# Performance work log

Hardware: AMD Instinct MI355X
Metric: run time of the kernel (lower is better)

## Reference

```python
import jax, jax.numpy as jnp
import numpy as np

QDEPTH = 20
WIDTH = HEIGHT = 28
PIXELS = WIDTH * HEIGHT          # 784
WIRES = 10                        # ceil(log2(784))
BATCH = 8192


def setup_inputs() -> dict:
    key = jax.random.key(0)
    k1, k2, k3, k4 = jax.random.split(key, 4)
    x = jax.random.normal(k1, (BATCH, 1, WIDTH, HEIGHT), jnp.float32)
    W = jax.random.normal(k2, (WIRES, PIXELS), jnp.float32) / np.sqrt(PIXELS)
    b = jax.random.normal(k3, (WIRES,), jnp.float32) * 0.01
    qweights = jax.random.normal(k4, (QDEPTH, WIRES, 3), jnp.float32) * 0.4
    return {"x": x, "W": W, "b": b, "qweights": qweights}


def _apply_1q(state, gate, wire):
    """Apply a single-qubit gate. state: (B,)+(2,)*WIRES; gate: (2,2) or (B,2,2)."""
    ax = 1 + wire
    s = jnp.moveaxis(state, ax, 1)
    shp = s.shape
    s = s.reshape(shp[0], 2, -1)
    if gate.ndim == 2:
        s = jnp.einsum('ij,bjr->bir', gate, s)
    else:
        s = jnp.einsum('bij,bjr->bir', gate, s)
    return jnp.moveaxis(s.reshape(shp), 1, ax)


def _cnot(state, c, t):
    """CNOT with control c, target t on state (B,)+(2,)*WIRES."""
    s = jnp.moveaxis(state, (1 + c, 1 + t), (1, 2))
    # when control==1, flip target axis
    s = jnp.concatenate([s[:, :1], jnp.flip(s[:, 1:2], axis=2)], axis=1)
    return jnp.moveaxis(s, (1, 2), (1 + c, 1 + t))


def _ry_batched(theta):
    """theta: (B,) -> (B,2,2) complex RY gates."""
    c = jnp.cos(theta / 2)
    s = jnp.sin(theta / 2)
    g = jnp.stack([jnp.stack([c, -s], -1), jnp.stack([s, c], -1)], -2)
    return g.astype(jnp.complex64)


def _rot(phi, theta, omega):
    """PennyLane Rot(phi,theta,omega) = RZ(omega) RY(theta) RZ(phi), scalars -> (2,2)."""
    c = jnp.cos(theta / 2)
    s = jnp.sin(theta / 2)
    m00 = jnp.exp(-0.5j * (phi + omega)) * c
    m01 = -jnp.exp(0.5j * (phi - omega)) * s
    m10 = jnp.exp(-0.5j * (phi - omega)) * s
    m11 = jnp.exp(0.5j * (phi + omega)) * c
    return jnp.stack([jnp.stack([m00, m01]), jnp.stack([m10, m11])]).astype(jnp.complex64)


def _forward(x, W, b, qweights):
    B = x.shape[0]
    feat = x.reshape(B, -1)                       # b 1 w h -> b (w h)
    angles = feat @ W.T + b                       # linear_down -> (B, WIRES)

    # |0...0> statevector, wire 0 most significant (PennyLane convention)
    state = jnp.zeros((B,) + (2,) * WIRES, jnp.complex64)
    state = state.at[(slice(None),) + (0,) * WIRES].set(1.0)

    # AngleEmbedding, rotation='Y'
    for w in range(WIRES):
        state = _apply_1q(state, _ry_batched(angles[:, w]), w)

    # StronglyEntanglingLayers: per-layer Rot on every wire, then CNOT ring
    for l in range(QDEPTH):
        for w in range(WIRES):
            state = _apply_1q(state, _rot(qweights[l, w, 0], qweights[l, w, 1], qweights[l, w, 2]), w)
        r = (l % (WIRES - 1)) + 1                 # default PennyLane ranges
        for w in range(WIRES):
            state = _cnot(state, w, (w + r) % WIRES)

    sv = state.reshape(B, -1)
    probs = sv.real ** 2 + sv.imag ** 2           # qml.probs over all wires
    out = jnp.clip(probs[:, :PIXELS] * PIXELS, 0.0, 1.0)
    return out.reshape(B, 1, WIDTH, HEIGHT)


def reference(x, W, b, qweights):
    return _forward(x, W, b, qweights)
```

## Files before the change

kernel.cpp:

```cpp
#include <hip/hip_runtime.h>
#include <hip/hip_bf16.h>
#include <stdint.h>


#define NWIRES  10
#define DIM     1024
#define NLAYERS 20
#define NGATES  200
#define NPASS   100
#define PIXELS  784
#define BATCH   8192

typedef _Float16 f16;
typedef _Float16 f16x8 __attribute__((ext_vector_type(8)));
typedef float    f32x4 __attribute__((ext_vector_type(4)));
typedef float    f32x2 __attribute__((ext_vector_type(2)));

typedef const __attribute__((address_space(1))) void* gas1_t;
typedef __attribute__((address_space(3))) void*       las3_t;

__device__ __forceinline__ void gload_lds16(const void* g, void* l) {
  __builtin_amdgcn_global_load_lds((gas1_t)g, (las3_t)l, 16, 0, 0);
}

__global__ __launch_bounds__(256) void k_prep(const float* __restrict__ qw,
                                              float* __restrict__ plan_mat,
                                              unsigned* __restrict__ plan_idx,
                                              unsigned* __restrict__ plan_final) {
  __shared__ float gm[NGATES][8];
  const int tid = threadIdx.x;

  if (tid < NGATES) {
    float phi = qw[tid * 3 + 0], th = qw[tid * 3 + 1], om = qw[tid * 3 + 2];
    float s, c, sa, ca, sb, cb;
    sincosf(0.5f * th, &s, &c);
    sincosf(0.5f * (phi + om), &sa, &ca);
    sincosf(0.5f * (phi - om), &sb, &cb);
    gm[tid][0] = ca * c;  gm[tid][1] = sa * c;
    gm[tid][2] = cb * s;  gm[tid][3] = sb * s;
    gm[tid][4] = -cb * s; gm[tid][5] = sb * s;
    gm[tid][6] = ca * c;  gm[tid][7] = -sa * c;
  }
  __syncthreads();

  if (tid == 0) {
    unsigned rowA[NWIRES], invc[NWIRES];
    for (int i = 0; i < NWIRES; i++) { rowA[i] = 1u << i; invc[i] = 1u << i; }
    for (int lrev = 0; lrev < NLAYERS; lrev++) {
      int l = NLAYERS - 1 - lrev;
      int r = (l % (NWIRES - 1)) + 1;
      for (int w = NWIRES - 1; w >= 0; w--) {
        int c = w, t = (w + r) % NWIRES;
        int pc = 9 - c, pt = 9 - t;
        rowA[pt] ^= rowA[pc];
        invc[pc] ^= invc[pt];
      }
      for (int s = 0; s < 5; s++) {
        int w1 = 2 * s, w2 = 2 * s + 1;
        int p1 = 9 - w1, p2 = 9 - w2;
        unsigned u1 = rowA[p1], u2 = rowA[p2];
        unsigned m1 = invc[p1], m2 = invc[p2];
        unsigned b1 = u1 & (0u - u1);
        if (u2 & b1) u2 ^= u1;
        unsigned b2 = u2 & (0u - u2);
        if (u1 & b2) u1 ^= u2;
        unsigned bLo = (b1 < b2) ? b1 : b2;
        unsigned bHi = (b1 < b2) ? b2 : b1;
        unsigned* P = plan_idx + (size_t)(lrev * 5 + s) * 8;
        P[0] = bLo; P[1] = bHi; P[2] = u1; P[3] = u2;
        P[4] = b1;  P[5] = b2;  P[6] = m1; P[7] = m2;
      }
    }
    for (int p = 0; p < NWIRES; p++) plan_final[p] = invc[p];
  } else if (tid >= 100 && tid < 200) {
    int t = tid - 100;
    int lrev = t / 5, s = t % 5;
    int l = NLAYERS - 1 - lrev;
    int g1 = l * NWIRES + 2 * s, g2 = g1 + 1;
    float* K = plan_mat + (size_t)t * 64;
#pragma unroll
    for (int r = 0; r < 4; r++) {
#pragma unroll
      for (int c = 0; c < 4; c++) {
        int r1 = r >> 1, c1 = c >> 1, r2 = r & 1, c2 = c & 1;
        float ar = gm[g1][(r1 * 2 + c1) * 2], ai = gm[g1][(r1 * 2 + c1) * 2 + 1];
        float br = gm[g2][(r2 * 2 + c2) * 2], bi = gm[g2][(r2 * 2 + c2) * 2 + 1];
        float kr = ar * br - ai * bi;
        float ki = ar * bi + ai * br;
        float* e = K + (r * 4 + c) * 4;
        e[0] = kr; e[1] = kr; e[2] = -ki; e[3] = ki;
      }
    }
  }
}

__global__ __launch_bounds__(256) void k_main(const float* __restrict__ plan_mat,
                                              const unsigned* __restrict__ plan_idx,
                                              const unsigned* __restrict__ plan_final,
                                              const float* __restrict__ x,
                                              const float* __restrict__ W,
                                              const float* __restrict__ bias,
                                              f16* __restrict__ E,
                                              f16* __restrict__ Bt) {
  __shared__ f32x2 st[DIM];
  __shared__ float part[4][NWIRES];
  __shared__ float csh[NWIRES][2];

  const int tid = threadIdx.x;

  if (blockIdx.x < PIXELS) {
    const int col = blockIdx.x;

    for (int i = tid; i < DIM; i += 256)
      st[i] = (f32x2){i == col ? 1.f : 0.f, 0.f};
    __syncthreads();

    for (int t = 0; t < NPASS; t++) {
      const unsigned* P = plan_idx + (size_t)t * 8;
      const unsigned bLo = P[0], bHi = P[1], u1 = P[2], u2 = P[3];
      const unsigned pb1 = P[4], pb2 = P[5], m1 = P[6], m2 = P[7];
      const f32x4* Kp = (const f32x4*)(plan_mat + (size_t)t * 64);

      unsigned q  = (unsigned)tid;
      unsigned xx = ((q & ~(bLo - 1u)) << 1) | (q & (bLo - 1u));
      unsigned j0 = ((xx & ~(bHi - 1u)) << 1) | (xx & (bHi - 1u));
      unsigned j  = j0 ^ ((__popc(u1 & j0) & 1) ? pb1 : 0u)
                       ^ ((__popc(u2 & j0) & 1) ? pb2 : 0u);

      f32x2 v0 = st[j];
      f32x2 v1 = st[j ^ m2];
      f32x2 v2 = st[j ^ m1];
      f32x2 v3 = st[j ^ m1 ^ m2];
      f32x2 w0 = {v0.y, v0.x}, w1 = {v1.y, v1.x};
      f32x2 w2 = {v2.y, v2.x}, w3 = {v3.y, v3.x};

      f32x2 r0 = {0.f, 0.f}, r1 = {0.f, 0.f}, r2 = {0.f, 0.f}, r3 = {0.f, 0.f};
#define CM(rr, e, vv, ww)                         \
      { f32x4 kk = Kp[e];                         \
        rr += (f32x2){kk.x, kk.y} * (vv);         \
        rr += (f32x2){kk.z, kk.w} * (ww); }
      CM(r0, 0, v0, w0)  CM(r0, 1, v1, w1)  CM(r0, 2, v2, w2)  CM(r0, 3, v3, w3)
      CM(r1, 4, v0, w0)  CM(r1, 5, v1, w1)  CM(r1, 6, v2, w2)  CM(r1, 7, v3, w3)
      CM(r2, 8, v0, w0)  CM(r2, 9, v1, w1)  CM(r2, 10, v2, w2) CM(r2, 11, v3, w3)
      CM(r3, 12, v0, w0) CM(r3, 13, v1, w1) CM(r3, 14, v2, w2) CM(r3, 15, v3, w3)
#undef CM

      __syncthreads();
      st[j]           = r0;
      st[j ^ m2]      = r1;
      st[j ^ m1]      = r2;
      st[j ^ m1 ^ m2] = r3;
      __syncthreads();
    }

    unsigned invl[NWIRES];
#pragma unroll
    for (int p = 0; p < NWIRES; p++) invl[p] = plan_final[p];

    __align__(8) f16 re4[4], im4[4];
#pragma unroll
    for (int u = 0; u < 4; u++) {
      int i = tid * 4 + u;
      unsigned j = 0;
#pragma unroll
      for (int p = 0; p < NWIRES; p++)
        if ((i >> p) & 1) j ^= invl[p];
      f32x2 v = st[j];
      re4[u] = (f16)v.x;
      im4[u] = (f16)(-v.y);
    }
    *(uint2*)(&Bt[(size_t)(2 * col) * DIM + tid * 4])     = *(const uint2*)re4;
    *(uint2*)(&Bt[(size_t)(2 * col + 1) * DIM + tid * 4]) = *(const uint2*)im4;
    return;
  }

  const int b = blockIdx.x - PIXELS;
  const float* xr = x + (size_t)b * PIXELS;

  float acc[NWIRES];
#pragma unroll
  for (int w = 0; w < NWIRES; w++) acc[w] = 0.f;

  for (int k = tid; k < PIXELS; k += 256) {
    float xv = xr[k];
#pragma unroll
    for (int w = 0; w < NWIRES; w++) acc[w] = fmaf(xv, W[w * PIXELS + k], acc[w]);
  }

#pragma unroll
  for (int w = 0; w < NWIRES; w++) {
    float v = acc[w];
#pragma unroll
    for (int off = 32; off > 0; off >>= 1) v += __shfl_xor(v, off, 64);
    acc[w] = v;
  }

  const int wv = tid >> 6, ln = tid & 63;
  if (ln == 0) {
#pragma unroll
    for (int w = 0; w < NWIRES; w++) part[wv][w] = acc[w];
  }
  __syncthreads();
  if (tid < NWIRES) {
    float a = part[0][tid] + part[1][tid] + part[2][tid] + part[3][tid] + bias[tid];
    float s, c;
    sincosf(0.5f * a, &s, &c);
    csh[tid][0] = c;
    csh[tid][1] = s;
  }
  __syncthreads();

  __align__(8) f16 e4[4];
#pragma unroll
  for (int u = 0; u < 4; u++) {
    int i = tid * 4 + u;
    float pr = 1.f;
#pragma unroll
    for (int w = 0; w < NWIRES; w++) pr *= csh[w][(i >> (9 - w)) & 1];
    e4[u] = (f16)pr;
  }
  *(uint2*)(&E[(size_t)b * DIM + tid * 4]) = *(const uint2*)e4;
}

__global__ __launch_bounds__(256) void k_gemm(const f16* __restrict__ E,
                                              const f16* __restrict__ Bt,
                                              float* __restrict__ out) {
  __shared__ __align__(16) f16 As[128 * 64];
  __shared__ __align__(16) f16 Bs[128 * 64];

  const int tid = threadIdx.x;
  const int wv = tid >> 6, ln = tid & 63;
  const int wr = wv >> 1, wc = wv & 1;

  const int bid = blockIdx.x;
  const int swz = (bid & 7) * 104 + (bid >> 3);
  const int mt  = swz / 13, nt = swz % 13;
  const int m0  = mt * 128;
  const int n0  = nt * 128;

  f32x4 acc[4][4];
#pragma unroll
  for (int a = 0; a < 4; a++)
#pragma unroll
    for (int q = 0; q < 4; q++) acc[a][q] = (f32x4){0.f, 0.f, 0.f, 0.f};

  for (int kt = 0; kt < 16; kt++) {
#pragma unroll
    for (int r = 0; r < 4; r++) {
      int ub  = (r * 4 + wv) * 64;
      int u   = ub + ln;
      int row = u >> 3;
      int cb  = (u & 7) * 16;
      const char* gA = (const char*)E  + ((size_t)(m0 + row) * 2048) + kt * 128 + cb;
      const char* gB = (const char*)Bt + ((size_t)(n0 + row) * 2048) + kt * 128 + cb;
      gload_lds16(gA, (char*)As + (size_t)ub * 16);
      gload_lds16(gB, (char*)Bs + (size_t)ub * 16);
    }
    __syncthreads();

#pragma unroll
    for (int ks = 0; ks < 2; ks++) {
      f16x8 af[4], bf[4];
#pragma unroll
      for (int mi = 0; mi < 4; mi++)
        af[mi] = *(const f16x8*)&As[(wr * 64 + mi * 16 + (ln & 15)) * 64 + ks * 32 + (ln >> 4) * 8];
#pragma unroll
      for (int ni = 0; ni < 4; ni++)
        bf[ni] = *(const f16x8*)&Bs[(wc * 64 + ni * 16 + (ln & 15)) * 64 + ks * 32 + (ln >> 4) * 8];
#pragma unroll
      for (int mi = 0; mi < 4; mi++)
#pragma unroll
        for (int ni = 0; ni < 4; ni++)
          acc[mi][ni] = __builtin_amdgcn_mfma_f32_16x16x32_f16(af[mi], bf[ni], acc[mi][ni], 0, 0, 0);
    }
    __syncthreads();
  }

#pragma unroll
  for (int mi = 0; mi < 4; mi++) {
#pragma unroll
    for (int ni = 0; ni < 4; ni++) {
      int nbase = n0 + wc * 64 + ni * 16 + (ln & 15);
      int p = nbase >> 1;
      bool even = (ln & 1) == 0;
#pragma unroll
      for (int r = 0; r < 4; r++) {
        float v = acc[mi][ni][r];
        float o = __shfl_xor(v, 1, 64);
        if (even && p < PIXELS) {
          int m = m0 + wr * 64 + mi * 16 + (ln >> 4) * 4 + r;
          float s2 = (v * v + o * o) * (float)PIXELS;
          out[(size_t)m * PIXELS + p] = fminf(fmaxf(s2, 0.f), 1.f);
        }
      }
    }
  }
}

extern "C" void kernel_launch(void* const* d_in, const int* in_sizes, int n_in,
                              void* d_out, int out_size, void* d_ws, size_t ws_size,
                              hipStream_t stream) {
  const float* x    = (const float*)d_in[0];
  const float* W    = (const float*)d_in[1];
  const float* bias = (const float*)d_in[2];
  const float* qw   = (const float*)d_in[3];
  float* out        = (float*)d_out;

  char* ws = (char*)d_ws;
  f16* E  = (f16*)(ws);
  f16* Bt = (f16*)(ws + (size_t)16 * 1024 * 1024);
  float*    plan_mat   = (float*)(ws + (size_t)20 * 1024 * 1024);
  unsigned* plan_idx   = (unsigned*)(ws + (size_t)20 * 1024 * 1024 + 65536);
  unsigned* plan_final = (unsigned*)(ws + (size_t)20 * 1024 * 1024 + 131072);

  k_prep<<<dim3(1), dim3(256), 0, stream>>>(qw, plan_mat, plan_idx, plan_final);
  k_main<<<dim3(PIXELS + BATCH), dim3(256), 0, stream>>>(plan_mat, plan_idx,
                                                         plan_final, x, W, bias,
                                                         E, Bt);
  k_gemm<<<dim3(832), dim3(256), 0, stream>>>(E, Bt, out);
}
```

Baseline: 146.7 us.

## Retile GEMM to double-buffered 256x256 tiles and drop redundant gate-loop barrier

Rewrites the probability GEMM to use 256x256 output tiles with 512 threads. It double-buffers the global-to-LDS loads so the next K slice streams in while MFMAs run, and raises MFMA wave priority during the compute phase. It also removes one __syncthreads in the gate-application loop of k_main, relying on each thread owning a disjoint group of four amplitudes. The larger tiles cut global traffic per FLOP, but the grid shrinks to 224 blocks (fewer than the CU count) at 128KB of LDS per block, and the N range now reads padded Bt rows that are masked out at store.

Result: faster. 143.1 us (-2.5%).

```diff
diff --git a/kernel.cpp b/kernel.cpp
--- a/kernel.cpp
+++ b/kernel.cpp
@@ -145,7 +145,6 @@
       CM(r3, 12, v0, w0) CM(r3, 13, v1, w1) CM(r3, 14, v2, w2) CM(r3, 15, v3, w3)
 #undef CM
 
-      __syncthreads();
       st[j]           = r0;
       st[j ^ m2]      = r1;
       st[j ^ m1]      = r2;
@@ -222,73 +221,91 @@
   *(uint2*)(&E[(size_t)b * DIM + tid * 4]) = *(const uint2*)e4;
 }
 
-__global__ __launch_bounds__(256) void k_gemm(const f16* __restrict__ E,
-                                              const f16* __restrict__ Bt,
-                                              float* __restrict__ out) {
-  __shared__ __align__(16) f16 As[128 * 64];
-  __shared__ __align__(16) f16 Bs[128 * 64];
+__device__ __forceinline__ void g_stage(const f16* __restrict__ g, f16* l,
+                                        int tid, int row0, int kt) {
+#pragma unroll
+  for (int r = 0; r < 4; r++) {
+    int u = r * 512 + tid;
+    int row = u >> 3, c8 = u & 7;
+    gload_lds16((const char*)g + (size_t)(row0 + row) * 2048 + kt * 128 + c8 * 16,
+                (char*)l + (size_t)u * 16);
+  }
+}
+
+__global__ __launch_bounds__(512, 2) void k_gemm(const f16* __restrict__ E,
+                                                 const f16* __restrict__ Bt,
+                                                 float* __restrict__ out) {
+  __shared__ __align__(16) f16 As[2][256 * 64];
+  __shared__ __align__(16) f16 Bs[2][256 * 64];
 
   const int tid = threadIdx.x;
-  const int wv = tid >> 6, ln = tid & 63;
-  const int wr = wv >> 1, wc = wv & 1;
+  const int wid = tid >> 6, ln = tid & 63;
+  const int wm = wid >> 2, wn = wid & 3;
 
   const int bid = blockIdx.x;
-  const int swz = (bid & 7) * 104 + (bid >> 3);
-  const int mt  = swz / 13, nt = swz % 13;
-  const int m0  = mt * 128;
-  const int n0  = nt * 128;
-
-  f32x4 acc[4][4];
-#pragma unroll
-  for (int a = 0; a < 4; a++)
+  const int swz = (bid & 7) * 28 + (bid >> 3);
+  const int mt  = swz % 32, nt = swz / 32;
+  const int m0  = mt * 256;
+  const int n0  = nt * 256;
+
+  f32x4 acc[8][4];
+#pragma unroll
+  for (int a = 0; a < 8; a++)
 #pragma unroll
     for (int q = 0; q < 4; q++) acc[a][q] = (f32x4){0.f, 0.f, 0.f, 0.f};
 
-  for (int kt = 0; kt < 16; kt++) {
-#pragma unroll
-    for (int r = 0; r < 4; r++) {
-      int ub  = (r * 4 + wv) * 64;
-      int u   = ub + ln;
-      int row = u >> 3;
-      int cb  = (u & 7) * 16;
-      const char* gA = (const char*)E  + ((size_t)(m0 + row) * 2048) + kt * 128 + cb;
-      const char* gB = (const char*)Bt + ((size_t)(n0 + row) * 2048) + kt * 128 + cb;
-      gload_lds16(gA, (char*)As + (size_t)ub * 16);
-      gload_lds16(gB, (char*)Bs + (size_t)ub * 16);
-    }
+#define COMPUTE(buf)                                                            \
+  {                                                                             \
+    _Pragma("unroll")                                                           \
+    for (int kk = 0; kk < 2; kk++) {                                            \
+      f16x8 af[8], bf[4];                                                       \
+      _Pragma("unroll")                                                         \
+      for (int mi = 0; mi < 8; mi++)                                            \
+        af[mi] = *(const f16x8*)&As[buf][(wm * 128 + mi * 16 + (ln & 15)) * 64  \
+                                         + kk * 32 + (ln >> 4) * 8];            \
+      _Pragma("unroll")                                                         \
+      for (int ni = 0; ni < 4; ni++)                                            \
+        bf[ni] = *(const f16x8*)&Bs[buf][(wn * 64 + ni * 16 + (ln & 15)) * 64   \
+                                         + kk * 32 + (ln >> 4) * 8];            \
+      __builtin_amdgcn_s_setprio(1);                                            \
+      _Pragma("unroll")                                                         \
+      for (int mi = 0; mi < 8; mi++)                                            \
+        _Pragma("unroll")                                                       \
+        for (int ni = 0; ni < 4; ni++)                                          \
+          acc[mi][ni] = __builtin_amdgcn_mfma_f32_16x16x32_f16(                 \
+              af[mi], bf[ni], acc[mi][ni], 0, 0, 0);                            \
+      __builtin_amdgcn_s_setprio(0);                                            \
+    }                                                                           \
+  }
+
+  g_stage(E,  &As[0][0], tid, m0, 0);
+  g_stage(Bt, &Bs[0][0], tid, n0, 0);
+  __syncthreads();
+
+  int cur = 0;
+  for (int kt = 0; kt < 15; kt++) {
+    g_stage(E,  &As[cur ^ 1][0], tid, m0, kt + 1);
+    g_stage(Bt, &Bs[cur ^ 1][0], tid, n0, kt + 1);
+    COMPUTE(cur);
     __syncthreads();
-
-#pragma unroll
-    for (int ks = 0; ks < 2; ks++) {
-      f16x8 af[4], bf[4];
-#pragma unroll
-      for (int mi = 0; mi < 4; mi++)
-        af[mi] = *(const f16x8*)&As[(wr * 64 + mi * 16 + (ln & 15)) * 64 + ks * 32 + (ln >> 4) * 8];
-#pragma unroll
-      for (int ni = 0; ni < 4; ni++)
-        bf[ni] = *(const f16x8*)&Bs[(wc * 64 + ni * 16 + (ln & 15)) * 64 + ks * 32 + (ln >> 4) * 8];
-#pragma unroll
-      for (int mi = 0; mi < 4; mi++)
-#pragma unroll
-        for (int ni = 0; ni < 4; ni++)
-          acc[mi][ni] = __builtin_amdgcn_mfma_f32_16x16x32_f16(af[mi], bf[ni], acc[mi][ni], 0, 0, 0);
-    }
-    __syncthreads();
-  }
-
-#pragma unroll
-  for (int mi = 0; mi < 4; mi++) {
+    cur ^= 1;
+  }
+  COMPUTE(cur);
+#undef COMPUTE
+
+#pragma unroll
+  for (int mi = 0; mi < 8; mi++) {
 #pragma unroll
     for (int ni = 0; ni < 4; ni++) {
-      int nbase = n0 + wc * 64 + ni * 16 + (ln & 15);
-      int p = nbase >> 1;
+      int n = n0 + wn * 64 + ni * 16 + (ln & 15);
+      int p = n >> 1;
       bool even = (ln & 1) == 0;
 #pragma unroll
       for (int r = 0; r < 4; r++) {
         float v = acc[mi][ni][r];
         float o = __shfl_xor(v, 1, 64);
         if (even && p < PIXELS) {
-          int m = m0 + wr * 64 + mi * 16 + (ln >> 4) * 4 + r;
+          int m = m0 + wm * 128 + mi * 16 + (ln >> 4) * 4 + r;
           float s2 = (v * v + o * o) * (float)PIXELS;
           out[(size_t)m * PIXELS + p] = fminf(fmaxf(s2, 0.f), 1.f);
         }
@@ -317,5 +334,5 @@
   k_main<<<dim3(PIXELS + BATCH), dim3(256), 0, stream>>>(plan_mat, plan_idx,
                                                          plan_final, x, W, bias,
                                                          E, Bt);
-  k_gemm<<<dim3(832), dim3(256), 0, stream>>>(E, Bt, out);
-}
+  k_gemm<<<dim3(224), dim3(512), 0, stream>>>(E, Bt, out);
+}
```
